# Optimization experiments

Hardware: AMD Instinct MI355X
Metric: run time of the kernel (lower is better)

Reference implementation:

```python
import jax, jax.numpy as jnp
import numpy as np

B, T, C, HS = 8, 4096, 1024, 64
HALF = HS // 2
ROPE_BASE = 10000.0


def _rope_tables(t_len, half_dim, base=ROPE_BASE):
    inv_freq = base ** (-jnp.arange(half_dim, dtype=jnp.float32) / half_dim)
    freqs = jnp.arange(t_len, dtype=jnp.float32)[:, None] * inv_freq[None, :]  # (T, D/2)
    return jnp.cos(freqs), jnp.sin(freqs)


def apply_rope(x, cos, sin):
    # x: (B, T, D) with interleaved even/odd pairs; cos/sin: (T, D/2)
    x_even = x[..., ::2]
    x_odd = x[..., 1::2]
    r_even = x_even * cos[None] - x_odd * sin[None]
    r_odd = x_even * sin[None] + x_odd * cos[None]
    # re-interleave
    return jnp.stack([r_even, r_odd], axis=-1).reshape(x.shape)


def setup_inputs() -> dict:
    key = jax.random.key(0)
    kx, kq, kk, kv = jax.random.split(key, 4)
    s = 1.0 / np.sqrt(C)
    cos, sin = _rope_tables(T, HALF)
    return {
        "x": jax.random.normal(kx, (B, T, C), dtype=jnp.float32),
        "cos": cos,
        "sin": sin,
        "Wq": jax.random.normal(kq, (C, HS), dtype=jnp.float32) * s,
        "Wk": jax.random.normal(kk, (C, HS), dtype=jnp.float32) * s,
        "Wv": jax.random.normal(kv, (C, HS), dtype=jnp.float32) * s,
    }


def reference(x, cos, sin, Wq, Wk, Wv):
    # q/k/v projections (bias-free Linear)
    q = jnp.einsum('btc,cd->btd', x, Wq)
    k = jnp.einsum('btc,cd->btd', x, Wk)
    v = jnp.einsum('btc,cd->btd', x, Wv)
    q = apply_rope(q, cos, sin)
    k = apply_rope(k, cos, sin)
    t = x.shape[1]
    scale = 1.0 / jnp.sqrt(jnp.asarray(k.shape[-1], dtype=x.dtype))
    wei = jnp.einsum('bqd,bkd->bqk', q, k) * scale  # (B, T, T)
    causal = jnp.tril(jnp.ones((t, t), dtype=bool))
    wei = jnp.where(causal[None], wei, -jnp.inf)
    wei = jax.nn.softmax(wei, axis=-1)
    # dropout = 0.0 (eval mode)
    return jnp.einsum('bqk,bkd->bqd', wei, v)
```

## Files before the change

kernel.cpp:

```cpp
#include <hip/hip_runtime.h>
#include <hip/hip_bf16.h>

#define BB 8
#define TT 4096
#define CC 1024
#define HS 64

typedef __attribute__((ext_vector_type(8))) __bf16 bf16x8;
typedef __attribute__((ext_vector_type(4))) __bf16 bf16x4;
typedef __attribute__((ext_vector_type(4))) float f32x4;

static __device__ __forceinline__ unsigned pack_bf16(float a, float b) {
    unsigned short ua = __builtin_bit_cast(unsigned short, (__bf16)a);
    unsigned short ub = __builtin_bit_cast(unsigned short, (__bf16)b);
    return (unsigned)ua | ((unsigned)ub << 16);
}
static __device__ __forceinline__ unsigned pack_f16(float a, float b) {
    unsigned short ua = __builtin_bit_cast(unsigned short, (_Float16)a);
    unsigned short ub = __builtin_bit_cast(unsigned short, (_Float16)b);
    return (unsigned)ua | ((unsigned)ub << 16);
}
static __device__ __forceinline__ float h2f(unsigned short u) {
    return (float)__builtin_bit_cast(_Float16, u);
}

__global__ __launch_bounds__(256) void wprep_kernel(
    const float* __restrict__ Wq, const float* __restrict__ Wk,
    const float* __restrict__ Wv, __bf16* __restrict__ Wt)
{
    int i = blockIdx.x * 256 + threadIdx.x;
    int dr = i >> 10;
    int c  = i & 1023;
    int m  = dr >> 6;
    int d  = dr & 63;
    const float* src = (m == 0) ? Wq : ((m == 1) ? Wk : Wv);
    float v = src[(long)c * HS + d];
    if (m == 0) v *= 0.125f * 1.4426950408889634f;
    Wt[i] = (__bf16)v;
}

__global__ __launch_bounds__(256) void qkv_rope_kernel(
    const float* __restrict__ x,
    const float* __restrict__ cosT,
    const float* __restrict__ sinT,
    const __bf16* __restrict__ Wt,
    __bf16* __restrict__ Qo, __bf16* __restrict__ Ko, __bf16* __restrict__ Vo)
{
    __shared__ __bf16 xs[64][72];
    __shared__ __bf16 Wl[192][72];

    const int tid  = threadIdx.x;
    const int lane = tid & 63;
    const int w    = tid >> 6;
    const int col  = lane & 15;
    const int grp  = lane >> 4;
    const long rowbase = (long)blockIdx.x * 64;

    f32x4 acc[12];
#pragma unroll
    for (int i = 0; i < 12; i++) acc[i] = 0.0f;

    for (int ck = 0; ck < CC; ck += 64) {
        {
            int r = tid >> 2, c0 = (tid & 3) * 16;
            const float4* src = (const float4*)(x + (rowbase + r) * (long)CC + ck + c0);
#pragma unroll
            for (int i = 0; i < 4; i++) {
                float4 v = src[i];
                bf16x4 t;
                t[0] = (__bf16)v.x; t[1] = (__bf16)v.y;
                t[2] = (__bf16)v.z; t[3] = (__bf16)v.w;
                *(bf16x4*)&xs[r][c0 + i * 4] = t;
            }
        }
        {
#pragma unroll
            for (int i = 0; i < 6; i++) {
                int u = i * 256 + tid;
                int dr = u >> 3, cu = (u & 7) * 8;
                bf16x8 v = *(const bf16x8*)(Wt + (long)dr * CC + ck + cu);
                *(bf16x8*)&Wl[dr][cu] = v;
            }
        }
        __syncthreads();
#pragma unroll
        for (int s = 0; s < 2; s++) {
            bf16x8 a = *(const bf16x8*)&xs[w * 16 + col][s * 32 + grp * 8];
#pragma unroll
            for (int nf = 0; nf < 12; nf++) {
                bf16x8 b = *(const bf16x8*)&Wl[nf * 16 + col][s * 32 + grp * 8];
                acc[nf] = __builtin_amdgcn_mfma_f32_16x16x32_bf16(a, b, acc[nf], 0, 0, 0);
            }
        }
        __syncthreads();
    }

#pragma unroll
    for (int r = 0; r < 4; r++) {
        long grow = rowbase + w * 16 + grp * 4 + r;
        int t = (int)(grow & (TT - 1));
        const float* cp = cosT + (long)t * 32;
        const float* sp = sinT + (long)t * 32;
#pragma unroll
        for (int nf = 0; nf < 4; nf++) {
            int ii = nf * 8 + (col >> 1);
            float cs = cp[ii], sn = sp[ii];
            float sgn_sn = (col & 1) ? sn : -sn;
            float qv = acc[nf][r];
            float qp = __shfl_xor(qv, 1);
            float qo = qv * cs + qp * sgn_sn;
            float kv = acc[nf + 4][r];
            float kp = __shfl_xor(kv, 1);
            float ko = kv * cs + kp * sgn_sn;
            long base = grow * HS + nf * 16 + col;
            Qo[base] = (__bf16)qo;
            Ko[base] = (__bf16)ko;
            xs[nf * 16 + col][w * 16 + grp * 4 + r] = (__bf16)acc[nf + 8][r];
        }
    }
    __syncthreads();
    {
        int d = tid >> 2, seg = tid & 3;
        int b  = (int)(rowbase >> 12);
        int t0 = (int)(rowbase & (TT - 1));
        bf16x8 v0 = *(const bf16x8*)&xs[d][seg * 16];
        bf16x8 v1 = *(const bf16x8*)&xs[d][seg * 16 + 8];
        __bf16* dst = Vo + ((size_t)b * 64 + d) * TT + t0 + seg * 16;
        *(bf16x8*)dst = v0;
        *(bf16x8*)(dst + 8) = v1;
    }
}

__global__ __launch_bounds__(256, 2) void attn_kernel(
    const __bf16* __restrict__ Q, const __bf16* __restrict__ K,
    const __bf16* __restrict__ Vt,
    _Float16* __restrict__ Opart, float* __restrict__ mlbuf)
{
    __shared__ __bf16 Kl[2][64 * 64];
    __shared__ __bf16 Vl[2][64 * 64];
    __shared__ __align__(16) unsigned char plds[4][2][2048];

    const int tid  = threadIdx.x;
    const int lane = tid & 63;
    const int col  = lane & 15;
    const int g    = lane >> 4;
    const int w    = tid >> 6;

    const int n = blockIdx.x;
    const int b = n & 7;
    const int j_ = n >> 3;
    int Qt, ch, j0, j1;
    if (j_ < 32) { Qt = 31 - j_; ch = 0; j0 = 0;      j1 = Qt + 1; }
    else         { Qt = j_ - 32; ch = 1; j0 = Qt + 1; j1 = 2 * Qt + 2; }

    const int qbase = Qt * 128 + w * 32;
    const size_t qgrow = (size_t)b * TT + qbase;
    bf16x8 qb[2][2];
#pragma unroll
    for (int sub = 0; sub < 2; sub++)
#pragma unroll
        for (int s = 0; s < 2; s++)
            qb[sub][s] = *(const bf16x8*)(Q + (qgrow + sub * 16 + col) * HS + s * 32 + g * 8);

    const int r0 = tid >> 3, c0 = tid & 7;
    const int r1 = r0 + 32;
    const __bf16* Kbase = K + (size_t)b * TT * HS;
    const __bf16* Vbase = Vt + (size_t)b * 64 * TT;

#define SWZ(row, cb) (((row) << 6) | (((cb) ^ ((row) & 7)) << 3))

    f32x4 acc[2][4];
#pragma unroll
    for (int sub = 0; sub < 2; sub++)
#pragma unroll
        for (int i = 0; i < 4; i++) acc[sub][i] = 0.f;
    float mrun[2] = { -3e38f, -3e38f };
    float lsum[2][4] = { {0.f,0.f,0.f,0.f}, {0.f,0.f,0.f,0.f} };

    const int sw = col & 7;

    bf16x8 sk0, sk1, sv0, sv1;
    auto stageLoad = [&](int j) {
        const __bf16* kp = Kbase + (size_t)(j * 64) * HS;
        sk0 = *(const bf16x8*)(kp + r0 * HS + c0 * 8);
        sk1 = *(const bf16x8*)(kp + r1 * HS + c0 * 8);
        const __bf16* vp = Vbase + j * 64;
        sv0 = *(const bf16x8*)(vp + (size_t)r0 * TT + c0 * 8);
        sv1 = *(const bf16x8*)(vp + (size_t)r1 * TT + c0 * 8);
    };
    auto stageWrite = [&](int buf) {
        *(bf16x8*)&Kl[buf][SWZ(r0, c0)] = sk0;
        *(bf16x8*)&Kl[buf][SWZ(r1, c0)] = sk1;
        *(bf16x8*)&Vl[buf][SWZ(r0, c0)] = sv0;
        *(bf16x8*)&Vl[buf][SWZ(r1, c0)] = sv1;
    };

    stageLoad(j0);
    stageWrite(0);
    __syncthreads();

    int cur = 0;
    for (int j = j0; j < j1; ++j) {
        const bool more = (j + 1 < j1);
        if (more) stageLoad(j + 1);
        __builtin_amdgcn_sched_barrier(0);

        bf16x8 kf[8];
#pragma unroll
        for (int nf = 0; nf < 4; nf++)
#pragma unroll
            for (int s = 0; s < 2; s++)
                kf[nf * 2 + s] = *(const bf16x8*)&Kl[cur][SWZ(nf * 16 + col, s * 4 + g)];

#pragma unroll
        for (int sub = 0; sub < 2; sub++) {
            if (j * 64 > qbase + sub * 16) continue;
            f32x4 sf[4];
#pragma unroll
            for (int i = 0; i < 4; i++) sf[i] = 0.f;
            __builtin_amdgcn_s_setprio(1);
#pragma unroll
            for (int s = 0; s < 2; s++)
#pragma unroll
                for (int nf = 0; nf < 4; nf++)
                    sf[nf] = __builtin_amdgcn_mfma_f32_16x16x32_bf16(kf[nf * 2 + s], qb[sub][s], sf[nf], 0, 0, 0);
            __builtin_amdgcn_s_setprio(0);
            if (j >= 2 * Qt) {
                const int qloc = qbase + sub * 16 + col;
#pragma unroll
                for (int nf = 0; nf < 4; nf++)
#pragma unroll
                    for (int r = 0; r < 4; r++)
                        if (j * 64 + nf * 16 + g * 4 + r > qloc) sf[nf][r] = -3e38f;
            }
            float fm[4];
#pragma unroll
            for (int f = 0; f < 4; f++)
                fm[f] = fmaxf(fmaxf(sf[f][0], sf[f][1]), fmaxf(sf[f][2], sf[f][3]));
            float mt = fmaxf(fmaxf(fm[0], fm[1]), fmaxf(fm[2], fm[3]));
            if (!__all(mt <= mrun[sub] + 8.0f)) {
                float mg = fmaxf(mt, __shfl_xor(mt, 16));
                mg = fmaxf(mg, __shfl_xor(mg, 32));
                float mn = fmaxf(mrun[sub], mg);
                float al = exp2f(mrun[sub] - mn);
                mrun[sub] = mn;
#pragma unroll
                for (int q = 0; q < 4; q++) lsum[sub][q] *= al;
#pragma unroll
                for (int nf = 0; nf < 4; nf++) acc[sub][nf] *= al;
            }
#pragma unroll
            for (int f = 0; f < 4; f++) {
                float p0 = exp2f(sf[f][0] - mrun[sub]);
                float p1 = exp2f(sf[f][1] - mrun[sub]);
                float p2 = exp2f(sf[f][2] - mrun[sub]);
                float p3 = exp2f(sf[f][3] - mrun[sub]);
                sf[f][0] = p0; sf[f][1] = p1; sf[f][2] = p2; sf[f][3] = p3;
                lsum[sub][0] += p0; lsum[sub][1] += p1;
                lsum[sub][2] += p2; lsum[sub][3] += p3;
            }
            unsigned char* pb = &plds[w][sub][0] + col * 128;
#pragma unroll
            for (int nf = 0; nf < 4; nf++) {
                uint2 val;
                val.x = pack_bf16(sf[nf][0], sf[nf][1]);
                val.y = pack_bf16(sf[nf][2], sf[nf][3]);
                *(uint2*)(pb + ((((nf * 2 + (g >> 1)) ^ sw) << 4) | ((g & 1) << 3))) = val;
            }
        }

        bf16x8 vf[8];
#pragma unroll
        for (int nf = 0; nf < 4; nf++)
#pragma unroll
            for (int s = 0; s < 2; s++)
                vf[nf * 2 + s] = *(const bf16x8*)&Vl[cur][SWZ(nf * 16 + col, s * 4 + g)];

#pragma unroll
        for (int sub = 0; sub < 2; sub++) {
            if (j * 64 > qbase + sub * 16) continue;
            unsigned char* pb = &plds[w][sub][0] + col * 128;
            __builtin_amdgcn_s_setprio(1);
#pragma unroll
            for (int s = 0; s < 2; s++) {
                bf16x8 pf = *(const bf16x8*)(pb + (((s * 4 + g) ^ sw) << 4));
#pragma unroll
                for (int nf = 0; nf < 4; nf++)
                    acc[sub][nf] = __builtin_amdgcn_mfma_f32_16x16x32_bf16(vf[nf * 2 + s], pf, acc[sub][nf], 0, 0, 0);
            }
            __builtin_amdgcn_s_setprio(0);
        }

        if (more) stageWrite(cur ^ 1);
        __syncthreads();
        cur ^= 1;
    }

    const size_t slot = (size_t)(b * 32 + Qt) * 2 + ch;
#pragma unroll
    for (int sub = 0; sub < 2; sub++) {
        float ls = (lsum[sub][0] + lsum[sub][1]) + (lsum[sub][2] + lsum[sub][3]);
        ls += __shfl_xor(ls, 16);
        ls += __shfl_xor(ls, 32);
        float rinv = (ls > 0.f) ? __builtin_amdgcn_rcpf(ls) : 0.f;
        const int rowg = w * 32 + sub * 16 + col;
        _Float16* prow = Opart + slot * 8192 + (size_t)rowg * 64;
#pragma unroll
        for (int nf = 0; nf < 4; nf++) {
            uint2 v;
            v.x = pack_f16(acc[sub][nf][0] * rinv, acc[sub][nf][1] * rinv);
            v.y = pack_f16(acc[sub][nf][2] * rinv, acc[sub][nf][3] * rinv);
            *(uint2*)(prow + nf * 16 + g * 4) = v;
        }
        if (g == 0) {
            float2 mv = make_float2(mrun[sub], ls);
            *(float2*)(mlbuf + (slot * 128 + rowg) * 2) = mv;
        }
    }
#undef SWZ
}

__global__ __launch_bounds__(256) void combine_kernel(
    const _Float16* __restrict__ Opart, const float* __restrict__ mlbuf,
    float* __restrict__ O)
{
    const int Qt = blockIdx.x;
    const int b  = blockIdx.y;
    const int row = threadIdx.x >> 1;
    const int seg = threadIdx.x & 1;
    const size_t slot0 = (size_t)(b * 32 + Qt) * 2;

    const float* p0 = mlbuf + ((slot0 + 0) * 128 + row) * 2;
    const float* p1 = mlbuf + ((slot0 + 1) * 128 + row) * 2;
    float m0 = p0[0], l0 = p0[1];
    float m1 = p1[0], l1 = p1[1];
    float M  = fmaxf(m0, m1);
    float w0 = l0 * exp2f(m0 - M);
    float w1 = l1 * exp2f(m1 - M);
    float rinv = 1.0f / (w0 + w1);
    w0 *= rinv; w1 *= rinv;

    const uint4* s0 = (const uint4*)(Opart + (slot0 + 0) * 8192 + (size_t)row * 64 + seg * 32);
    const uint4* s1 = (const uint4*)(Opart + (slot0 + 1) * 8192 + (size_t)row * 64 + seg * 32);
    float* dst = O + ((size_t)b * TT + Qt * 128 + row) * 64 + seg * 32;
#pragma unroll
    for (int i = 0; i < 4; i++) {
        uint4 a = s0[i], c = s1[i];
        float4 v;
        v.x = h2f((unsigned short)(a.x      )) * w0 + h2f((unsigned short)(c.x      )) * w1;
        v.y = h2f((unsigned short)(a.x >> 16)) * w0 + h2f((unsigned short)(c.x >> 16)) * w1;
        v.z = h2f((unsigned short)(a.y      )) * w0 + h2f((unsigned short)(c.y      )) * w1;
        v.w = h2f((unsigned short)(a.y >> 16)) * w0 + h2f((unsigned short)(c.y >> 16)) * w1;
        *(float4*)(dst + i * 8) = v;
        float4 u;
        u.x = h2f((unsigned short)(a.z      )) * w0 + h2f((unsigned short)(c.z      )) * w1;
        u.y = h2f((unsigned short)(a.z >> 16)) * w0 + h2f((unsigned short)(c.z >> 16)) * w1;
        u.z = h2f((unsigned short)(a.w      )) * w0 + h2f((unsigned short)(c.w      )) * w1;
        u.w = h2f((unsigned short)(a.w >> 16)) * w0 + h2f((unsigned short)(c.w >> 16)) * w1;
        *(float4*)(dst + i * 8 + 4) = u;
    }
}

extern "C" void kernel_launch(void* const* d_in, const int* in_sizes, int n_in,
                              void* d_out, int out_size, void* d_ws, size_t ws_size,
                              hipStream_t stream)
{
    const float* x    = (const float*)d_in[0];
    const float* cosT = (const float*)d_in[1];
    const float* sinT = (const float*)d_in[2];
    const float* Wq   = (const float*)d_in[3];
    const float* Wk   = (const float*)d_in[4];
    const float* Wv   = (const float*)d_in[5];
    float* out = (float*)d_out;

    __bf16* Qb = (__bf16*)d_ws;
    __bf16* Kb = Qb + (size_t)BB * TT * HS;
    __bf16* Vb = Kb + (size_t)BB * TT * HS;
    __bf16* Wt = Vb + (size_t)BB * TT * HS;

    const size_t base_bytes = (size_t)3 * BB * TT * HS * 2 + 192 * 1024 * 2;
    _Float16* Opart = (_Float16*)((char*)d_ws + ((base_bytes + 255) & ~(size_t)255));
    float* mlbuf = (float*)(Opart + (size_t)512 * 8192);

    wprep_kernel<<<(192 * 1024) / 256, 256, 0, stream>>>(Wq, Wk, Wv, Wt);
    qkv_rope_kernel<<<(BB * TT) / 64, 256, 0, stream>>>(x, cosT, sinT, Wt, Qb, Kb, Vb);
    attn_kernel<<<512, 256, 0, stream>>>(Qb, Kb, Vb, Opart, mlbuf);
    combine_kernel<<<dim3(32, 8), 256, 0, stream>>>(Opart, mlbuf, out);
}
```

Before: 101.7 us.

## Software-pipeline QK^T of next tile with softmax/PV of previous tile

Restructures the attention main loop so the QK^T MFMAs for tile j are issued before the softmax and PV MFMAs for tile j-1, using two ping-ponged score register sets. The V buffer becomes triple-buffered so the previous tile's V stays resident while the next one is written, and the P scratch shrinks to one slot per wave. The goal is to overlap MFMA work with exp/max VALU work and hide dependency latency. In exchange, score register pressure doubles, which risks spills or lower occupancy under launch_bounds(256,2), and the code gains prologue and epilogue complexity.

```diff
diff --git a/kernel.cpp b/kernel.cpp
--- a/kernel.cpp
+++ b/kernel.cpp
@@ -137,8 +137,8 @@
     _Float16* __restrict__ Opart, float* __restrict__ mlbuf)
 {
     __shared__ __bf16 Kl[2][64 * 64];
-    __shared__ __bf16 Vl[2][64 * 64];
-    __shared__ __align__(16) unsigned char plds[4][2][2048];
+    __shared__ __bf16 Vl[3][64 * 64];
+    __shared__ __align__(16) unsigned char plds[4][2048];
 
     const int tid  = threadIdx.x;
     const int lane = tid & 63;
@@ -146,8 +146,8 @@
     const int g    = lane >> 4;
     const int w    = tid >> 6;
 
-    const int n = blockIdx.x;
-    const int b = n & 7;
+    const int n  = blockIdx.x;
+    const int b  = n & 7;
     const int j_ = n >> 3;
     int Qt, ch, j0, j1;
     if (j_ < 32) { Qt = 31 - j_; ch = 0; j0 = 0;      j1 = Qt + 1; }
@@ -177,6 +177,7 @@
     float mrun[2] = { -3e38f, -3e38f };
     float lsum[2][4] = { {0.f,0.f,0.f,0.f}, {0.f,0.f,0.f,0.f} };
 
+    unsigned char* pbase = plds[w] + col * 128;
     const int sw = col & 7;
 
     bf16x8 sk0, sk1, sv0, sv1;
@@ -188,55 +189,62 @@
         sv0 = *(const bf16x8*)(vp + (size_t)r0 * TT + c0 * 8);
         sv1 = *(const bf16x8*)(vp + (size_t)r1 * TT + c0 * 8);
     };
-    auto stageWrite = [&](int buf) {
-        *(bf16x8*)&Kl[buf][SWZ(r0, c0)] = sk0;
-        *(bf16x8*)&Kl[buf][SWZ(r1, c0)] = sk1;
-        *(bf16x8*)&Vl[buf][SWZ(r0, c0)] = sv0;
-        *(bf16x8*)&Vl[buf][SWZ(r1, c0)] = sv1;
-    };
-
-    stageLoad(j0);
-    stageWrite(0);
-    __syncthreads();
-
-    int cur = 0;
-    for (int j = j0; j < j1; ++j) {
-        const bool more = (j + 1 < j1);
-        if (more) stageLoad(j + 1);
-        __builtin_amdgcn_sched_barrier(0);
-
+    auto stageWriteK = [&](int kb) {
+        *(bf16x8*)&Kl[kb][SWZ(r0, c0)] = sk0;
+        *(bf16x8*)&Kl[kb][SWZ(r1, c0)] = sk1;
+    };
+    auto stageWriteV = [&](int vb) {
+        *(bf16x8*)&Vl[vb][SWZ(r0, c0)] = sv0;
+        *(bf16x8*)&Vl[vb][SWZ(r1, c0)] = sv1;
+    };
+
+    f32x4 sfA[2][4], sfB[2][4];
+
+    auto qkPhase = [&](int jv, f32x4 (&SF)[2][4]) {
         bf16x8 kf[8];
 #pragma unroll
         for (int nf = 0; nf < 4; nf++)
 #pragma unroll
             for (int s = 0; s < 2; s++)
-                kf[nf * 2 + s] = *(const bf16x8*)&Kl[cur][SWZ(nf * 16 + col, s * 4 + g)];
-
+                kf[nf * 2 + s] = *(const bf16x8*)&Kl[jv & 1][SWZ(nf * 16 + col, s * 4 + g)];
+        __builtin_amdgcn_s_setprio(1);
 #pragma unroll
         for (int sub = 0; sub < 2; sub++) {
-            if (j * 64 > qbase + sub * 16) continue;
-            f32x4 sf[4];
-#pragma unroll
-            for (int i = 0; i < 4; i++) sf[i] = 0.f;
-            __builtin_amdgcn_s_setprio(1);
+            if (jv * 64 > qbase + sub * 16) continue;
+#pragma unroll
+            for (int i = 0; i < 4; i++) SF[sub][i] = 0.f;
 #pragma unroll
             for (int s = 0; s < 2; s++)
 #pragma unroll
                 for (int nf = 0; nf < 4; nf++)
-                    sf[nf] = __builtin_amdgcn_mfma_f32_16x16x32_bf16(kf[nf * 2 + s], qb[sub][s], sf[nf], 0, 0, 0);
-            __builtin_amdgcn_s_setprio(0);
-            if (j >= 2 * Qt) {
+                    SF[sub][nf] = __builtin_amdgcn_mfma_f32_16x16x32_bf16(kf[nf * 2 + s], qb[sub][s], SF[sub][nf], 0, 0, 0);
+        }
+        __builtin_amdgcn_s_setprio(0);
+    };
+
+    auto finPhase = [&](int jv, f32x4 (&SF)[2][4]) {
+        const int vb = jv % 3;
+        bf16x8 vf[8];
+#pragma unroll
+        for (int nf = 0; nf < 4; nf++)
+#pragma unroll
+            for (int s = 0; s < 2; s++)
+                vf[nf * 2 + s] = *(const bf16x8*)&Vl[vb][SWZ(nf * 16 + col, s * 4 + g)];
+#pragma unroll
+        for (int sub = 0; sub < 2; sub++) {
+            if (jv * 64 > qbase + sub * 16) continue;
+            if (jv >= 2 * Qt) {
                 const int qloc = qbase + sub * 16 + col;
 #pragma unroll
                 for (int nf = 0; nf < 4; nf++)
 #pragma unroll
                     for (int r = 0; r < 4; r++)
-                        if (j * 64 + nf * 16 + g * 4 + r > qloc) sf[nf][r] = -3e38f;
+                        if (jv * 64 + nf * 16 + g * 4 + r > qloc) SF[sub][nf][r] = -3e38f;
             }
             float fm[4];
 #pragma unroll
             for (int f = 0; f < 4; f++)
-                fm[f] = fmaxf(fmaxf(sf[f][0], sf[f][1]), fmaxf(sf[f][2], sf[f][3]));
+                fm[f] = fmaxf(fmaxf(SF[sub][f][0], SF[sub][f][1]), fmaxf(SF[sub][f][2], SF[sub][f][3]));
             float mt = fmaxf(fmaxf(fm[0], fm[1]), fmaxf(fm[2], fm[3]));
             if (!__all(mt <= mrun[sub] + 8.0f)) {
                 float mg = fmaxf(mt, __shfl_xor(mt, 16));
@@ -251,50 +259,77 @@
             }
 #pragma unroll
             for (int f = 0; f < 4; f++) {
-                float p0 = exp2f(sf[f][0] - mrun[sub]);
-                float p1 = exp2f(sf[f][1] - mrun[sub]);
-                float p2 = exp2f(sf[f][2] - mrun[sub]);
-                float p3 = exp2f(sf[f][3] - mrun[sub]);
-                sf[f][0] = p0; sf[f][1] = p1; sf[f][2] = p2; sf[f][3] = p3;
+                float p0 = exp2f(SF[sub][f][0] - mrun[sub]);
+                float p1 = exp2f(SF[sub][f][1] - mrun[sub]);
+                float p2 = exp2f(SF[sub][f][2] - mrun[sub]);
+                float p3 = exp2f(SF[sub][f][3] - mrun[sub]);
+                SF[sub][f][0] = p0; SF[sub][f][1] = p1;
+                SF[sub][f][2] = p2; SF[sub][f][3] = p3;
                 lsum[sub][0] += p0; lsum[sub][1] += p1;
                 lsum[sub][2] += p2; lsum[sub][3] += p3;
             }
-            unsigned char* pb = &plds[w][sub][0] + col * 128;
 #pragma unroll
             for (int nf = 0; nf < 4; nf++) {
                 uint2 val;
-                val.x = pack_bf16(sf[nf][0], sf[nf][1]);
-                val.y = pack_bf16(sf[nf][2], sf[nf][3]);
-                *(uint2*)(pb + ((((nf * 2 + (g >> 1)) ^ sw) << 4) | ((g & 1) << 3))) = val;
-            }
-        }
-
-        bf16x8 vf[8];
-#pragma unroll
-        for (int nf = 0; nf < 4; nf++)
-#pragma unroll
-            for (int s = 0; s < 2; s++)
-                vf[nf * 2 + s] = *(const bf16x8*)&Vl[cur][SWZ(nf * 16 + col, s * 4 + g)];
-
-#pragma unroll
-        for (int sub = 0; sub < 2; sub++) {
-            if (j * 64 > qbase + sub * 16) continue;
-            unsigned char* pb = &plds[w][sub][0] + col * 128;
+                val.x = pack_bf16(SF[sub][nf][0], SF[sub][nf][1]);
+                val.y = pack_bf16(SF[sub][nf][2], SF[sub][nf][3]);
+                *(uint2*)(pbase + ((((nf * 2 + (g >> 1)) ^ sw) << 4) | ((g & 1) << 3))) = val;
+            }
             __builtin_amdgcn_s_setprio(1);
 #pragma unroll
             for (int s = 0; s < 2; s++) {
-                bf16x8 pf = *(const bf16x8*)(pb + (((s * 4 + g) ^ sw) << 4));
+                bf16x8 pf = *(const bf16x8*)(pbase + (((s * 4 + g) ^ sw) << 4));
 #pragma unroll
                 for (int nf = 0; nf < 4; nf++)
                     acc[sub][nf] = __builtin_amdgcn_mfma_f32_16x16x32_bf16(vf[nf * 2 + s], pf, acc[sub][nf], 0, 0, 0);
             }
             __builtin_amdgcn_s_setprio(0);
         }
-
-        if (more) stageWrite(cur ^ 1);
+    };
+
+    auto iterStep = [&](int jv, f32x4 (&SFq)[2][4], f32x4 (&SFf)[2][4]) {
+        const bool more = (jv + 1 < j1);
+        if (more) stageLoad(jv + 1);
+        __builtin_amdgcn_sched_barrier(0);
+        qkPhase(jv, SFq);
+        finPhase(jv - 1, SFf);
+        if (more) {
+            stageWriteK((jv + 1) & 1);
+            stageWriteV((jv + 1) % 3);
+        }
         __syncthreads();
-        cur ^= 1;
-    }
+    };
+
+    stageLoad(j0);
+    stageWriteK(j0 & 1);
+    stageWriteV(j0 % 3);
+    __syncthreads();
+
+    {
+        const bool more = (j0 + 1 < j1);
+        if (more) stageLoad(j0 + 1);
+        __builtin_amdgcn_sched_barrier(0);
+        qkPhase(j0, sfA);
+        if (more) {
+            stageWriteK((j0 + 1) & 1);
+            stageWriteV((j0 + 1) % 3);
+        }
+        __syncthreads();
+    }
+
+    int jv = j0 + 1;
+    while (jv + 1 < j1) {
+        iterStep(jv, sfB, sfA);
+        iterStep(jv + 1, sfA, sfB);
+        jv += 2;
+    }
+    bool lastIsB = false;
+    if (jv < j1) {
+        iterStep(jv, sfB, sfA);
+        lastIsB = true;
+    }
+    if (lastIsB) finPhase(j1 - 1, sfB);
+    else         finPhase(j1 - 1, sfA);
 
     const size_t slot = (size_t)(b * 32 + Qt) * 2 + ch;
 #pragma unroll
```

After: 97.31 us. 1.05x faster.
